# Kernel tuning notes

Hardware: AMD Instinct MI355X
Metric: run time of the kernel (lower is better)

The kernel has to match this reference:

```python
import jax, jax.numpy as jnp
import numpy as np

N_USERS = 100_000
N_ITEMS = 50_000
N_NODES = N_USERS + N_ITEMS
D = 64
NUM_LAYERS = 3
N_INTER = 1_000_000  # interactions; symmetrized -> 2M directed edges
BATCH = 4096


def setup_inputs() -> dict:
    key = jax.random.key(0)
    k_u, k_i, k_r, k_c, k_uid, k_iid = jax.random.split(key, 6)
    user_embedding = jax.random.normal(k_u, (N_USERS, D), dtype=jnp.float32)
    item_embedding = jax.random.normal(k_i, (N_ITEMS, D), dtype=jnp.float32)

    # build symmetric normalized adjacency edges as in get_norm_adj_mat
    rng = np.random.default_rng(0)
    row = rng.integers(0, N_USERS, size=N_INTER)
    col = rng.integers(0, N_ITEMS, size=N_INTER) + N_USERS
    src = np.concatenate([row, col])
    dst = np.concatenate([col, row])
    deg = np.bincount(src, minlength=N_NODES).astype(np.float32)
    norm_deg = 1.0 / np.sqrt(np.where(deg == 0, 1.0, deg))
    edge_weight = (norm_deg[src] * norm_deg[dst]).astype(np.float32)
    edge_index = np.stack([src, dst]).astype(np.int64)

    user_id = jax.random.randint(k_uid, (BATCH,), 0, N_USERS)
    item_id = jax.random.randint(k_iid, (BATCH,), 0, N_ITEMS)
    return {
        "user_embedding": user_embedding,
        "item_embedding": item_embedding,
        "edge_weight": jnp.asarray(edge_weight),
        "edge_index": jnp.asarray(edge_index),
        "user_id": user_id,
        "item_id": item_id,
    }


def reference(user_embedding, item_embedding, edge_weight, edge_index, user_id, item_id):
    # ego embeddings: [N_NODES, D]
    x = jnp.concatenate([user_embedding, item_embedding], axis=0)
    src, dst = edge_index[0], edge_index[1]
    h = x
    acc = x  # running sum over layer outputs (incl. layer 0)
    for _ in range(NUM_LAYERS):
        # LightGCNConv: gather source, scale by edge weight, scatter-add to dest
        msg = h[src] * edge_weight[:, None]                       # [E, D]
        h = jax.ops.segment_sum(msg, dst, num_segments=N_NODES)   # [N, D]
        acc = acc + h
    final = acc / jnp.asarray(NUM_LAYERS + 1, dtype=x.dtype)      # mean over layers
    u_embed = final[:N_USERS][user_id]
    i_embed = final[N_USERS:][item_id]
    return (u_embed, i_embed)
```

## Files before the change

kernel.cpp:

```cpp
#include <hip/hip_runtime.h>

#define N_USERS 100000
#define N_NODES 150000
#define DIM 64
#define BATCH 4096
#define BSHIFT 9
#define BUCKET 512
#define NB 293
#define PAIRS_PER_BLK 8192
#define BUCKET_SLACK 2048

typedef unsigned short bf16_t;

static __device__ __forceinline__ float bf2f(bf16_t h) {
    return __uint_as_float(((unsigned)h) << 16);
}
static __device__ __forceinline__ bf16_t f2bf(float f) {
    unsigned u = __float_as_uint(f);
    return (bf16_t)((u + 0x7FFFu + ((u >> 16) & 1u)) >> 16);
}

__global__ void lgcn_bin_count(const int* __restrict__ row, const int* __restrict__ col,
                               int* __restrict__ blockhist, int EH) {
    __shared__ int h[4 * NB];
    for (int i = threadIdx.x; i < 4 * NB; i += blockDim.x) h[i] = 0;
    __syncthreads();
    int k = blockIdx.x;
    int wv = threadIdx.x >> 6;
    int* hw = h + wv * NB;
    int e0 = k * PAIRS_PER_BLK;
    int e1 = min(EH, e0 + PAIRS_PER_BLK);
    int nq = (e1 - e0) >> 2;
    const int4* r4 = (const int4*)(row + e0);
    const int4* c4 = (const int4*)(col + e0);
    for (int q = threadIdx.x; q < nq; q += blockDim.x) {
        int4 r = r4[q];
        int4 c = c4[q];
        atomicAdd(&hw[r.x >> BSHIFT], 1); atomicAdd(&hw[c.x >> BSHIFT], 1);
        atomicAdd(&hw[r.y >> BSHIFT], 1); atomicAdd(&hw[c.y >> BSHIFT], 1);
        atomicAdd(&hw[r.z >> BSHIFT], 1); atomicAdd(&hw[c.z >> BSHIFT], 1);
        atomicAdd(&hw[r.w >> BSHIFT], 1); atomicAdd(&hw[c.w >> BSHIFT], 1);
    }
    __syncthreads();
    for (int i = threadIdx.x; i < NB; i += blockDim.x)
        blockhist[k * NB + i] = h[i] + h[NB + i] + h[2 * NB + i] + h[3 * NB + i];
}

__global__ void lgcn_scan_blocks(int* __restrict__ blockhist, int* __restrict__ totals,
                                 int NB1) {
    __shared__ int bufA[128], bufB[128];
    int b = blockIdx.x;
    int i = threadIdx.x;
    int v = (i < NB1) ? blockhist[i * NB + b] : 0;
    bufA[i] = v;
    __syncthreads();
    int* cur = bufA; int* nxt = bufB;
    for (int off = 1; off < 128; off <<= 1) {
        nxt[i] = (i >= off) ? cur[i] + cur[i - off] : cur[i];
        __syncthreads();
        int* t = cur; cur = nxt; nxt = t;
    }
    if (i < NB1) blockhist[i * NB + b] = cur[i] - v;
    if (i == 127) totals[b] = cur[127];
}

__global__ void lgcn_scan_buckets(const int* __restrict__ totals,
                                  int* __restrict__ bucket_base) {
    __shared__ int bufA[512], bufB[512];
    int i = threadIdx.x;
    int v = (i < NB) ? totals[i] : 0;
    bufA[i] = v;
    __syncthreads();
    int* cur = bufA; int* nxt = bufB;
    for (int off = 1; off < 512; off <<= 1) {
        nxt[i] = (i >= off) ? cur[i] + cur[i - off] : cur[i];
        __syncthreads();
        int* t = cur; cur = nxt; nxt = t;
    }
    if (i < NB) bucket_base[i] = cur[i] - v;
    if (i == 511) bucket_base[NB] = cur[511];
}

__global__ void lgcn_bin_scatter(const int* __restrict__ row, const int* __restrict__ col,
                                 const int* __restrict__ blockhist,
                                 const int* __restrict__ bucket_base,
                                 int* __restrict__ binned, int EH) {
    __shared__ int cur[NB];
    int k = blockIdx.x;
    for (int i = threadIdx.x; i < NB; i += blockDim.x)
        cur[i] = bucket_base[i] + blockhist[k * NB + i];
    __syncthreads();
    int e0 = k * PAIRS_PER_BLK;
    int e1 = min(EH, e0 + PAIRS_PER_BLK);
    int nq = (e1 - e0) >> 2;
    const int4* r4 = (const int4*)(row + e0);
    const int4* c4 = (const int4*)(col + e0);
    for (int q = threadIdx.x; q < nq; q += blockDim.x) {
        int4 r = r4[q];
        int4 c = c4[q];
        int rr[4] = { r.x, r.y, r.z, r.w };
        int cc[4] = { c.x, c.y, c.z, c.w };
#pragma unroll
        for (int j = 0; j < 4; ++j) {
            int p1 = atomicAdd(&cur[cc[j] >> BSHIFT], 1);
            binned[p1] = ((cc[j] & (BUCKET - 1)) << 18) | rr[j];
            int p2 = atomicAdd(&cur[rr[j] >> BSHIFT], 1);
            binned[p2] = ((rr[j] & (BUCKET - 1)) << 18) | cc[j];
        }
    }
}

__global__ void __launch_bounds__(BUCKET)
lgcn_build_csr(const int* __restrict__ bucket_base, const int* __restrict__ binned,
               int4* __restrict__ nodeinfo, int* __restrict__ packed) {
    __shared__ int hist[BUCKET], sA[BUCKET], sB[BUCKET], cur[BUCKET];
    int b = blockIdx.x;
    int tid = threadIdx.x;
    hist[tid] = 0;
    __syncthreads();
    int e0 = bucket_base[b], e1 = bucket_base[b + 1];
    for (int j = e0 + tid; j < e1; j += BUCKET)
        atomicAdd(&hist[binned[j] >> 18], 1);
    __syncthreads();
    int deg = hist[tid];
    int degp = (deg + 3) & ~3;
    sA[tid] = degp;
    __syncthreads();
    int* c_ = sA; int* n_ = sB;
    for (int off = 1; off < BUCKET; off <<= 1) {
        n_[tid] = (tid >= off) ? c_[tid] + c_[tid - off] : c_[tid];
        __syncthreads();
        int* t = c_; c_ = n_; n_ = t;
    }
    int pbase = (e0 & ~3) + BUCKET_SLACK * b;
    int start = pbase + (c_[tid] - degp);
    cur[tid] = start;
    int node = (b << BSHIFT) + tid;
    if (node < N_NODES) {
        float da = (deg == 0) ? 1.0f : (float)deg;
        float sq = sqrtf(da);
        int4 ni;
        ni.x = start;
        ni.y = deg;
        ni.z = __float_as_int(1.0f / sq);
        ni.w = __float_as_int(sq);
        nodeinfo[node] = ni;
    }
    __syncthreads();
    for (int j = e0 + tid; j < e1; j += BUCKET) {
        int w = binned[j];
        int pos = atomicAdd(&cur[w >> 18], 1);
        packed[pos] = w & 0x3FFFF;
    }
}


__global__ void lgcn_init_g0(const float* __restrict__ ue, const float* __restrict__ ie,
                             const int4* __restrict__ nodeinfo, bf16_t* __restrict__ g0) {
    int t = blockIdx.x * blockDim.x + threadIdx.x;
    const int nT = N_NODES * (DIM / 4);
    if (t >= nT) return;
    int n = t >> 4;
    const int nU = N_USERS * (DIM / 4);
    float4 x = (t < nU) ? ((const float4*)ue)[t] : ((const float4*)ie)[t - nU];
    float nm = __int_as_float(nodeinfo[n].z);
    ushort4 o;
    o.x = f2bf(x.x * nm); o.y = f2bf(x.y * nm);
    o.z = f2bf(x.z * nm); o.w = f2bf(x.w * nm);
    ((ushort4*)g0)[t] = o;
}

static __device__ __forceinline__ float4
gather_sum(const bf16_t* __restrict__ g, const int* __restrict__ packed,
           int start, int deg, int grp, int c) {
    float4 acc = make_float4(0.f, 0.f, 0.f, 0.f);
    for (int o = 4 * grp; o < deg; o += 16) {
        int4 e4 = *(const int4*)(packed + start + o);
        int s0 = min((unsigned)e4.x, (unsigned)(N_NODES - 1));
        int s1 = min((unsigned)e4.y, (unsigned)(N_NODES - 1));
        int s2 = min((unsigned)e4.z, (unsigned)(N_NODES - 1));
        int s3 = min((unsigned)e4.w, (unsigned)(N_NODES - 1));
        ushort4 v0 = ((const ushort4*)(g + (size_t)s0 * DIM))[c];
        ushort4 v1 = ((const ushort4*)(g + (size_t)s1 * DIM))[c];
        ushort4 v2 = ((const ushort4*)(g + (size_t)s2 * DIM))[c];
        ushort4 v3 = ((const ushort4*)(g + (size_t)s3 * DIM))[c];
        float w0 = (o + 0 < deg) ? 1.0f : 0.0f;
        float w1 = (o + 1 < deg) ? 1.0f : 0.0f;
        float w2 = (o + 2 < deg) ? 1.0f : 0.0f;
        float w3 = (o + 3 < deg) ? 1.0f : 0.0f;
        acc.x = fmaf(bf2f(v0.x), w0, acc.x); acc.y = fmaf(bf2f(v0.y), w0, acc.y);
        acc.z = fmaf(bf2f(v0.z), w0, acc.z); acc.w = fmaf(bf2f(v0.w), w0, acc.w);
        acc.x = fmaf(bf2f(v1.x), w1, acc.x); acc.y = fmaf(bf2f(v1.y), w1, acc.y);
        acc.z = fmaf(bf2f(v1.z), w1, acc.z); acc.w = fmaf(bf2f(v1.w), w1, acc.w);
        acc.x = fmaf(bf2f(v2.x), w2, acc.x); acc.y = fmaf(bf2f(v2.y), w2, acc.y);
        acc.z = fmaf(bf2f(v2.z), w2, acc.z); acc.w = fmaf(bf2f(v2.w), w2, acc.w);
        acc.x = fmaf(bf2f(v3.x), w3, acc.x); acc.y = fmaf(bf2f(v3.y), w3, acc.y);
        acc.z = fmaf(bf2f(v3.z), w3, acc.z); acc.w = fmaf(bf2f(v3.w), w3, acc.w);
    }
    return acc;
}

__global__ void __launch_bounds__(256)
lgcn_pull(const bf16_t* __restrict__ g, const int4* __restrict__ nodeinfo,
          const int* __restrict__ packed, bf16_t* __restrict__ gn) {
    int n = blockIdx.x * 4 + (threadIdx.x >> 6);
    if (n >= N_NODES) return;
    int lane = threadIdx.x & 63;
    int grp = lane >> 4;
    int c = lane & 15;
    int4 ni = nodeinfo[n];
    float4 acc = gather_sum(g, packed, ni.x, ni.y, grp, c);
#pragma unroll
    for (int off = 16; off < 64; off <<= 1) {
        acc.x += __shfl_xor(acc.x, off, 64);
        acc.y += __shfl_xor(acc.y, off, 64);
        acc.z += __shfl_xor(acc.z, off, 64);
        acc.w += __shfl_xor(acc.w, off, 64);
    }
    if (lane < 16) {
        float nm = __int_as_float(ni.z);
        float s2 = nm * nm;
        ushort4 o;
        o.x = f2bf(acc.x * s2); o.y = f2bf(acc.y * s2);
        o.z = f2bf(acc.z * s2); o.w = f2bf(acc.w * s2);
        ((ushort4*)(gn + (size_t)n * DIM))[c] = o;
    }
}

__global__ void __launch_bounds__(256)
lgcn_final(const float* __restrict__ ue, const float* __restrict__ ie,
           const bf16_t* __restrict__ g1, const bf16_t* __restrict__ g2,
           const int4* __restrict__ nodeinfo, const int* __restrict__ packed,
           const int* __restrict__ uid, const int* __restrict__ iid,
           float* __restrict__ out) {
    int slot = blockIdx.x * 4 + (threadIdx.x >> 6);
    if (slot >= 2 * BATCH) return;
    int lane = threadIdx.x & 63;
    int grp = lane >> 4;
    int c = lane & 15;
    int isItem = slot >= BATCH;
    int b = isItem ? (slot - BATCH) : slot;
    int node = isItem ? (N_USERS + iid[b]) : uid[b];
    int4 ni = nodeinfo[node];
    float4 acc = gather_sum(g2, packed, ni.x, ni.y, grp, c);
#pragma unroll
    for (int off = 16; off < 64; off <<= 1) {
        acc.x += __shfl_xor(acc.x, off, 64);
        acc.y += __shfl_xor(acc.y, off, 64);
        acc.z += __shfl_xor(acc.z, off, 64);
        acc.w += __shfl_xor(acc.w, off, 64);
    }
    if (lane < 16) {
        const float* xb = isItem ? (ie + (size_t)(node - N_USERS) * DIM)
                                 : (ue + (size_t)node * DIM);
        float4 x = ((const float4*)xb)[c];
        ushort4 a1 = ((const ushort4*)(g1 + (size_t)node * DIM))[c];
        ushort4 a2 = ((const ushort4*)(g2 + (size_t)node * DIM))[c];
        float rn = __int_as_float(ni.w);
        float nm = __int_as_float(ni.z);
        float4 r;
        r.x = 0.25f * (x.x + rn * (bf2f(a1.x) + bf2f(a2.x)) + nm * acc.x);
        r.y = 0.25f * (x.y + rn * (bf2f(a1.y) + bf2f(a2.y)) + nm * acc.y);
        r.z = 0.25f * (x.z + rn * (bf2f(a1.z) + bf2f(a2.z)) + nm * acc.z);
        r.w = 0.25f * (x.w + rn * (bf2f(a1.w) + bf2f(a2.w)) + nm * acc.w);
        ((float4*)(out + (size_t)slot * DIM))[c] = r;
    }
}


extern "C" void kernel_launch(void* const* d_in, const int* in_sizes, int n_in,
                              void* d_out, int out_size, void* d_ws, size_t ws_size,
                              hipStream_t stream) {
    const float* ue  = (const float*)d_in[0];
    const float* ie  = (const float*)d_in[1];
    const int*   ei  = (const int*)d_in[3];
    const int*   uid = (const int*)d_in[4];
    const int*   iid = (const int*)d_in[5];
    float* out = (float*)d_out;

    const int E  = in_sizes[2];
    const int EH = E / 2;
    const int* row = ei;
    const int* col = ei + E;

    const int NB1 = (EH + PAIRS_PER_BLK - 1) / PAIRS_PER_BLK;

    char* p = (char*)d_ws;
    size_t off = 0;
    auto carve = [&](size_t bytes) -> char* {
        char* r = p + off;
        off += (bytes + 255) & ~(size_t)255;
        return r;
    };
    const size_t nodeBf16 = (size_t)N_NODES * DIM * sizeof(bf16_t);
    bf16_t* gA        = (bf16_t*)carve(nodeBf16);
    bf16_t* gB        = (bf16_t*)carve(nodeBf16);
    int4*   nodeinfo  = (int4*)carve((size_t)N_NODES * sizeof(int4));
    int*    blockhist = (int*)carve((size_t)128 * NB * sizeof(int));
    int*    totals    = (int*)carve((size_t)NB * sizeof(int));
    int*    bucketbase= (int*)carve((size_t)(NB + 1) * sizeof(int));
    int*    binned    = (int*)carve((size_t)E * sizeof(int));
    int*    packed    = (int*)carve((size_t)(E + BUCKET_SLACK * NB + 4) * sizeof(int));
    (void)ws_size;

    lgcn_bin_count<<<NB1, 256, 0, stream>>>(row, col, blockhist, EH);
    lgcn_scan_blocks<<<NB, 128, 0, stream>>>(blockhist, totals, NB1);
    lgcn_scan_buckets<<<1, 512, 0, stream>>>(totals, bucketbase);
    lgcn_bin_scatter<<<NB1, 256, 0, stream>>>(row, col, blockhist, bucketbase, binned, EH);
    lgcn_build_csr<<<NB, BUCKET, 0, stream>>>(bucketbase, binned, nodeinfo, packed);

    lgcn_init_g0<<<(N_NODES * (DIM / 4) + 255) / 256, 256, 0, stream>>>(ue, ie, nodeinfo, gA);

    const int pullGrid = (N_NODES + 3) / 4;
    lgcn_pull<<<pullGrid, 256, 0, stream>>>(gA, nodeinfo, packed, gB);
    lgcn_pull<<<pullGrid, 256, 0, stream>>>(gB, nodeinfo, packed, gA);
    lgcn_final<<<(2 * BATCH + 3) / 4, 256, 0, stream>>>(
        ue, ie, gB, gA, nodeinfo, packed, uid, iid, out);
}
```

Measured before the change: 239.4 us.

## Fuse edge binning into one pass with fixed-capacity buckets and padded sentinel gathers

Replaces the count/scan-blocks/scan-buckets/scatter sequence with a single binning kernel. Each block counts locally, then reserves space in fixed-capacity per-bucket regions through global atomics, which removes two scan kernels and a second read of the edge list. CSR padding slots now point to a zeroed sentinel node, so the gather loop drops its clamps and masking multiplies. The cost is a larger workspace, and correctness depends on no bucket exceeding its fixed capacity; edge order within a bucket also becomes nondeterministic.

After: 238.9 us (median of 2 runs). No clear change (-0.2%).

```diff
diff --git a/kernel.cpp b/kernel.cpp
--- a/kernel.cpp
+++ b/kernel.cpp
@@ -8,7 +8,8 @@
 #define BUCKET 512
 #define NB 293
 #define PAIRS_PER_BLK 8192
-#define BUCKET_SLACK 2048
+#define CAPSHIFT 14
+#define CAP (1 << CAPSHIFT)
 
 typedef unsigned short bf16_t;
 
@@ -20,9 +21,10 @@
     return (bf16_t)((u + 0x7FFFu + ((u >> 16) & 1u)) >> 16);
 }
 
-__global__ void lgcn_bin_count(const int* __restrict__ row, const int* __restrict__ col,
-                               int* __restrict__ blockhist, int EH) {
+__global__ void lgcn_bin(const int* __restrict__ row, const int* __restrict__ col,
+                         int* __restrict__ cursor, int* __restrict__ binned, int EH) {
     __shared__ int h[4 * NB];
+    __shared__ int basecur[NB];
     for (int i = threadIdx.x; i < 4 * NB; i += blockDim.x) h[i] = 0;
     __syncthreads();
     int k = blockIdx.x;
@@ -42,59 +44,13 @@
         atomicAdd(&hw[r.w >> BSHIFT], 1); atomicAdd(&hw[c.w >> BSHIFT], 1);
     }
     __syncthreads();
-    for (int i = threadIdx.x; i < NB; i += blockDim.x)
-        blockhist[k * NB + i] = h[i] + h[NB + i] + h[2 * NB + i] + h[3 * NB + i];
-}
-
-__global__ void lgcn_scan_blocks(int* __restrict__ blockhist, int* __restrict__ totals,
-                                 int NB1) {
-    __shared__ int bufA[128], bufB[128];
-    int b = blockIdx.x;
-    int i = threadIdx.x;
-    int v = (i < NB1) ? blockhist[i * NB + b] : 0;
-    bufA[i] = v;
-    __syncthreads();
-    int* cur = bufA; int* nxt = bufB;
-    for (int off = 1; off < 128; off <<= 1) {
-        nxt[i] = (i >= off) ? cur[i] + cur[i - off] : cur[i];
-        __syncthreads();
-        int* t = cur; cur = nxt; nxt = t;
-    }
-    if (i < NB1) blockhist[i * NB + b] = cur[i] - v;
-    if (i == 127) totals[b] = cur[127];
-}
-
-__global__ void lgcn_scan_buckets(const int* __restrict__ totals,
-                                  int* __restrict__ bucket_base) {
-    __shared__ int bufA[512], bufB[512];
-    int i = threadIdx.x;
-    int v = (i < NB) ? totals[i] : 0;
-    bufA[i] = v;
-    __syncthreads();
-    int* cur = bufA; int* nxt = bufB;
-    for (int off = 1; off < 512; off <<= 1) {
-        nxt[i] = (i >= off) ? cur[i] + cur[i - off] : cur[i];
-        __syncthreads();
-        int* t = cur; cur = nxt; nxt = t;
-    }
-    if (i < NB) bucket_base[i] = cur[i] - v;
-    if (i == 511) bucket_base[NB] = cur[511];
-}
-
-__global__ void lgcn_bin_scatter(const int* __restrict__ row, const int* __restrict__ col,
-                                 const int* __restrict__ blockhist,
-                                 const int* __restrict__ bucket_base,
-                                 int* __restrict__ binned, int EH) {
-    __shared__ int cur[NB];
-    int k = blockIdx.x;
-    for (int i = threadIdx.x; i < NB; i += blockDim.x)
-        cur[i] = bucket_base[i] + blockhist[k * NB + i];
-    __syncthreads();
-    int e0 = k * PAIRS_PER_BLK;
-    int e1 = min(EH, e0 + PAIRS_PER_BLK);
-    int nq = (e1 - e0) >> 2;
-    const int4* r4 = (const int4*)(row + e0);
-    const int4* c4 = (const int4*)(col + e0);
+    for (int i = threadIdx.x; i < NB; i += blockDim.x) {
+        int tot = h[i] + h[NB + i] + h[2 * NB + i] + h[3 * NB + i];
+        int base = i << CAPSHIFT;
+        if (tot) base += atomicAdd(&cursor[i], tot);
+        basecur[i] = base;
+    }
+    __syncthreads();
     for (int q = threadIdx.x; q < nq; q += blockDim.x) {
         int4 r = r4[q];
         int4 c = c4[q];
@@ -102,23 +58,24 @@
         int cc[4] = { c.x, c.y, c.z, c.w };
 #pragma unroll
         for (int j = 0; j < 4; ++j) {
-            int p1 = atomicAdd(&cur[cc[j] >> BSHIFT], 1);
+            int p1 = atomicAdd(&basecur[cc[j] >> BSHIFT], 1);
             binned[p1] = ((cc[j] & (BUCKET - 1)) << 18) | rr[j];
-            int p2 = atomicAdd(&cur[rr[j] >> BSHIFT], 1);
+            int p2 = atomicAdd(&basecur[rr[j] >> BSHIFT], 1);
             binned[p2] = ((rr[j] & (BUCKET - 1)) << 18) | cc[j];
         }
     }
 }
 
 __global__ void __launch_bounds__(BUCKET)
-lgcn_build_csr(const int* __restrict__ bucket_base, const int* __restrict__ binned,
+lgcn_build_csr(const int* __restrict__ cursor, const int* __restrict__ binned,
                int4* __restrict__ nodeinfo, int* __restrict__ packed) {
     __shared__ int hist[BUCKET], sA[BUCKET], sB[BUCKET], cur[BUCKET];
     int b = blockIdx.x;
     int tid = threadIdx.x;
     hist[tid] = 0;
     __syncthreads();
-    int e0 = bucket_base[b], e1 = bucket_base[b + 1];
+    int e0 = b << CAPSHIFT;
+    int e1 = e0 + cursor[b];
     for (int j = e0 + tid; j < e1; j += BUCKET)
         atomicAdd(&hist[binned[j] >> 18], 1);
     __syncthreads();
@@ -132,8 +89,7 @@
         __syncthreads();
         int* t = c_; c_ = n_; n_ = t;
     }
-    int pbase = (e0 & ~3) + BUCKET_SLACK * b;
-    int start = pbase + (c_[tid] - degp);
+    int start = e0 + (c_[tid] - degp);
     cur[tid] = start;
     int node = (b << BSHIFT) + tid;
     if (node < N_NODES) {
@@ -152,14 +108,23 @@
         int pos = atomicAdd(&cur[w >> 18], 1);
         packed[pos] = w & 0x3FFFF;
     }
+    for (int kk = deg; kk < degp; ++kk)
+        packed[start + kk] = N_NODES;
 }
 
 
 __global__ void lgcn_init_g0(const float* __restrict__ ue, const float* __restrict__ ie,
-                             const int4* __restrict__ nodeinfo, bf16_t* __restrict__ g0) {
+                             const int4* __restrict__ nodeinfo,
+                             bf16_t* __restrict__ g0, bf16_t* __restrict__ g1) {
     int t = blockIdx.x * blockDim.x + threadIdx.x;
     const int nT = N_NODES * (DIM / 4);
-    if (t >= nT) return;
+    if (t >= nT) {
+        if (t < nT + 16)
+            ((ushort4*)g0)[nT + (t - nT)] = make_ushort4(0, 0, 0, 0);
+        else if (t < nT + 32)
+            ((ushort4*)g1)[nT + (t - nT - 16)] = make_ushort4(0, 0, 0, 0);
+        return;
+    }
     int n = t >> 4;
     const int nU = N_USERS * (DIM / 4);
     float4 x = (t < nU) ? ((const float4*)ue)[t] : ((const float4*)ie)[t - nU];
@@ -176,26 +141,18 @@
     float4 acc = make_float4(0.f, 0.f, 0.f, 0.f);
     for (int o = 4 * grp; o < deg; o += 16) {
         int4 e4 = *(const int4*)(packed + start + o);
-        int s0 = min((unsigned)e4.x, (unsigned)(N_NODES - 1));
-        int s1 = min((unsigned)e4.y, (unsigned)(N_NODES - 1));
-        int s2 = min((unsigned)e4.z, (unsigned)(N_NODES - 1));
-        int s3 = min((unsigned)e4.w, (unsigned)(N_NODES - 1));
-        ushort4 v0 = ((const ushort4*)(g + (size_t)s0 * DIM))[c];
-        ushort4 v1 = ((const ushort4*)(g + (size_t)s1 * DIM))[c];
-        ushort4 v2 = ((const ushort4*)(g + (size_t)s2 * DIM))[c];
-        ushort4 v3 = ((const ushort4*)(g + (size_t)s3 * DIM))[c];
-        float w0 = (o + 0 < deg) ? 1.0f : 0.0f;
-        float w1 = (o + 1 < deg) ? 1.0f : 0.0f;
-        float w2 = (o + 2 < deg) ? 1.0f : 0.0f;
-        float w3 = (o + 3 < deg) ? 1.0f : 0.0f;
-        acc.x = fmaf(bf2f(v0.x), w0, acc.x); acc.y = fmaf(bf2f(v0.y), w0, acc.y);
-        acc.z = fmaf(bf2f(v0.z), w0, acc.z); acc.w = fmaf(bf2f(v0.w), w0, acc.w);
-        acc.x = fmaf(bf2f(v1.x), w1, acc.x); acc.y = fmaf(bf2f(v1.y), w1, acc.y);
-        acc.z = fmaf(bf2f(v1.z), w1, acc.z); acc.w = fmaf(bf2f(v1.w), w1, acc.w);
-        acc.x = fmaf(bf2f(v2.x), w2, acc.x); acc.y = fmaf(bf2f(v2.y), w2, acc.y);
-        acc.z = fmaf(bf2f(v2.z), w2, acc.z); acc.w = fmaf(bf2f(v2.w), w2, acc.w);
-        acc.x = fmaf(bf2f(v3.x), w3, acc.x); acc.y = fmaf(bf2f(v3.y), w3, acc.y);
-        acc.z = fmaf(bf2f(v3.z), w3, acc.z); acc.w = fmaf(bf2f(v3.w), w3, acc.w);
+        ushort4 v0 = ((const ushort4*)(g + (size_t)e4.x * DIM))[c];
+        ushort4 v1 = ((const ushort4*)(g + (size_t)e4.y * DIM))[c];
+        ushort4 v2 = ((const ushort4*)(g + (size_t)e4.z * DIM))[c];
+        ushort4 v3 = ((const ushort4*)(g + (size_t)e4.w * DIM))[c];
+        acc.x += bf2f(v0.x); acc.y += bf2f(v0.y);
+        acc.z += bf2f(v0.z); acc.w += bf2f(v0.w);
+        acc.x += bf2f(v1.x); acc.y += bf2f(v1.y);
+        acc.z += bf2f(v1.z); acc.w += bf2f(v1.w);
+        acc.x += bf2f(v2.x); acc.y += bf2f(v2.y);
+        acc.z += bf2f(v2.z); acc.w += bf2f(v2.w);
+        acc.x += bf2f(v3.x); acc.y += bf2f(v3.y);
+        acc.z += bf2f(v3.z); acc.w += bf2f(v3.w);
     }
     return acc;
 }
@@ -282,6 +239,7 @@
     const int EH = E / 2;
     const int* row = ei;
     const int* col = ei + E;
+    (void)E;
 
     const int NB1 = (EH + PAIRS_PER_BLK - 1) / PAIRS_PER_BLK;
 
@@ -292,24 +250,21 @@
         off += (bytes + 255) & ~(size_t)255;
         return r;
     };
-    const size_t nodeBf16 = (size_t)N_NODES * DIM * sizeof(bf16_t);
-    bf16_t* gA        = (bf16_t*)carve(nodeBf16);
-    bf16_t* gB        = (bf16_t*)carve(nodeBf16);
-    int4*   nodeinfo  = (int4*)carve((size_t)N_NODES * sizeof(int4));
-    int*    blockhist = (int*)carve((size_t)128 * NB * sizeof(int));
-    int*    totals    = (int*)carve((size_t)NB * sizeof(int));
-    int*    bucketbase= (int*)carve((size_t)(NB + 1) * sizeof(int));
-    int*    binned    = (int*)carve((size_t)E * sizeof(int));
-    int*    packed    = (int*)carve((size_t)(E + BUCKET_SLACK * NB + 4) * sizeof(int));
+    const size_t nodeBf16 = (size_t)(N_NODES + 1) * DIM * sizeof(bf16_t);
+    bf16_t* gA       = (bf16_t*)carve(nodeBf16);
+    bf16_t* gB       = (bf16_t*)carve(nodeBf16);
+    int4*   nodeinfo = (int4*)carve((size_t)N_NODES * sizeof(int4));
+    int*    cursor   = (int*)carve((size_t)NB * sizeof(int));
+    int*    binned   = (int*)carve((size_t)NB * CAP * sizeof(int));
+    int*    packed   = (int*)carve((size_t)NB * CAP * sizeof(int));
     (void)ws_size;
 
-    lgcn_bin_count<<<NB1, 256, 0, stream>>>(row, col, blockhist, EH);
-    lgcn_scan_blocks<<<NB, 128, 0, stream>>>(blockhist, totals, NB1);
-    lgcn_scan_buckets<<<1, 512, 0, stream>>>(totals, bucketbase);
-    lgcn_bin_scatter<<<NB1, 256, 0, stream>>>(row, col, blockhist, bucketbase, binned, EH);
-    lgcn_build_csr<<<NB, BUCKET, 0, stream>>>(bucketbase, binned, nodeinfo, packed);
-
-    lgcn_init_g0<<<(N_NODES * (DIM / 4) + 255) / 256, 256, 0, stream>>>(ue, ie, nodeinfo, gA);
+    hipMemsetAsync(cursor, 0, (size_t)NB * sizeof(int), stream);
+    lgcn_bin<<<NB1, 256, 0, stream>>>(row, col, cursor, binned, EH);
+    lgcn_build_csr<<<NB, BUCKET, 0, stream>>>(cursor, binned, nodeinfo, packed);
+
+    lgcn_init_g0<<<(N_NODES * (DIM / 4) + 32 + 255) / 256, 256, 0, stream>>>(
+        ue, ie, nodeinfo, gA, gB);
 
     const int pullGrid = (N_NODES + 3) / 4;
     lgcn_pull<<<pullGrid, 256, 0, stream>>>(gA, nodeinfo, packed, gB);
```
